# Optimization experiments

Hardware: AMD Instinct MI355X
Metric: run time of the kernel (lower is better)

## Reference

```python
import jax, jax.numpy as jnp
import numpy as np

B, L, D, K = 16, 2048, 128, 8192
NUM_RQ_STEPS = 1


def _nearest(residual, codebook):
    # residual: [B,L,D], codebook: [K,D]
    d2 = (
        jnp.sum(residual * residual, axis=-1, keepdims=True)  # [B,L,1]
        - 2.0 * jnp.einsum('bld,kd->blk', residual, codebook)  # [B,L,K]
        + jnp.sum(codebook * codebook, axis=-1)  # [K]
    )
    idx = jnp.argmin(d2, axis=-1)  # [B,L]
    return codebook[idx], idx  # gather: [B,L,D]


def setup_inputs() -> dict:
    key = jax.random.key(0)
    k1, k2 = jax.random.split(key)
    z_e = jax.random.normal(k1, (B, L, D), dtype=jnp.float32)
    codebook = jax.random.normal(k2, (K, D), dtype=jnp.float32)
    return {"z_e": z_e, "codebook": codebook}


def reference(z_e, codebook):
    # apply_codebook(z_e, code_sg=True): codebook is stop-gradiented,
    # residual quantization over NUM_RQ_STEPS, straight-through on output.
    cb = jax.lax.stop_gradient(codebook)
    residual = z_e
    z_q = jnp.zeros_like(z_e)
    idx_list = []
    for _ in range(NUM_RQ_STEPS):
        q, idx = _nearest(residual, cb)
        z_q = z_q + q
        residual = residual - q
        idx_list.append(idx)
    indices = jnp.stack(idx_list, axis=-1)  # [B,L,num_rq_steps]
    # straight-through estimator (code_sg=True): grads flow to z_e, not codebook
    z_q = z_e + jax.lax.stop_gradient(z_q - z_e)
    return z_q, indices
```

## Files before the change

### kernel.cpp

```cpp
#include <hip/hip_runtime.h>


#define M_TOK  32768
#define DIM    128
#define KCODES 8192
#define BM     64
#define NT     (KCODES / 256)
#define MARGIN 0.10f

typedef _Float16 half8v __attribute__((ext_vector_type(8)));
typedef float float4v __attribute__((ext_vector_type(4)));

union H2U { _Float16 h; unsigned short u; };
__device__ __forceinline__ unsigned short f2h_bits(_Float16 h) {
  H2U c; c.h = h; return c.u;
}

__device__ __forceinline__ void gload_lds16(const void* g, void* l) {
  __builtin_amdgcn_global_load_lds(
      (const __attribute__((address_space(1))) unsigned int*)g,
      (__attribute__((address_space(3))) unsigned int*)l, 16, 0, 0);
}

#define CNORM_OFF  (KCODES * 256)
#define QCNT_OFF   (CNORM_OFF + KCODES * 4)
#define QTOK_OFF   (QCNT_OFF + 64)
#define KMIN_OFF   (QTOK_OFF + M_TOK * 4)

__global__ __launch_bounds__(256) void prep_kernel(
    const float* __restrict__ cb, unsigned short* __restrict__ Cs,
    float* __restrict__ cnorm, int* __restrict__ qcnt) {
  if (blockIdx.x == 0 && threadIdx.x == 0) *qcnt = 0;
  const int k = blockIdx.x * 4 + (threadIdx.x >> 6);
  const int lane = threadIdx.x & 63;
  const float2 v = ((const float2*)(cb + (size_t)k * DIM))[lane];
  float s = v.x * v.x + v.y * v.y;
  #pragma unroll
  for (int off = 32; off > 0; off >>= 1) s += __shfl_down(s, off);
  if (lane == 0) cnorm[k] = s;
  ushort2 hi;
  hi.x = f2h_bits((_Float16)v.x);
  hi.y = f2h_bits((_Float16)v.y);
  *(ushort2*)(Cs + (size_t)k * 128 + lane * 2) = hi;
}

__global__ __launch_bounds__(256, 2) void vq_mfma_kernel(
    const float* __restrict__ ze, const unsigned short* __restrict__ Cs,
    const float* __restrict__ cnorm, const float* __restrict__ cb,
    int* __restrict__ qcnt, int* __restrict__ qtok,
    unsigned long long* __restrict__ kmin,
    float* __restrict__ out_zq, float* __restrict__ out_idx) {
  __shared__ char lds[49152];
  char* const As = lds;
  char* const Bs = lds + 16384;

  const int tid = threadIdx.x;
  const int wn = tid >> 6;
  const int lane = tid & 63;
  const int quad = lane >> 4;
  const int l15 = lane & 15;
  const int m0 = blockIdx.x * BM;

  int loffC[4];
  #pragma unroll
  for (int c = 0; c < 4; ++c) {
    const int r = c * 16 + (lane >> 2);
    const int s = lane & 3;
    const int seg = s ^ ((r >> 1) & 3);
    loffC[c] = (wn * 64 + r) * 256 + seg * 16;
  }
  int boff[4];
  #pragma unroll
  for (int j = 0; j < 4; ++j) {
    const int n = j * 16 + l15;
    boff[j] = n * 64 + ((quad ^ ((n >> 1) & 3)) << 4);
  }
  char* const BsW = Bs + wn * 8192;

  {
    const int r = tid >> 2;
    const int qh = tid & 3;
    const float* zrow = ze + (size_t)(m0 + r) * DIM + qh * 32;
    char* arow = As + r * 256;
    const int rx = r & 7;
    #pragma unroll
    for (int i = 0; i < 8; ++i) {
      const float4 v = *(const float4*)(zrow + i * 4);
      ushort4 hh;
      hh.x = f2h_bits((_Float16)v.x);
      hh.y = f2h_bits((_Float16)v.y);
      hh.z = f2h_bits((_Float16)v.z);
      hh.w = f2h_bits((_Float16)v.w);
      const int c = qh * 32 + i * 4;
      *(ushort4*)(arow + ((((c >> 3) ^ rx) << 4) | ((c & 7) << 1))) = hh;
    }
  }
  __syncthreads();

  half8v ahi[4][4];
  #pragma unroll
  for (int ks = 0; ks < 4; ++ks)
    #pragma unroll
    for (int i = 0; i < 4; ++i) {
      const int m = i * 16 + l15;
      const int kslot = ks * 4 + quad;
      ahi[ks][i] = *(const half8v*)(As + m * 256 + ((kslot ^ (m & 7)) << 4));
    }

  float bestv[16], secv[16], idxv[16];
  #pragma unroll
  for (int s = 0; s < 16; ++s) {
    bestv[s] = 3.4e38f; secv[s] = 3.4e38f; idxv[s] = 0.f;
  }

  for (int nt = 0; nt < NT; ++nt) {
    const char* const tile = (const char*)Cs + (size_t)nt * 65536;
    float cnv[4];
    #pragma unroll
    for (int j = 0; j < 4; ++j)
      cnv[j] = cnorm[nt * 256 + wn * 64 + j * 16 + l15];

    float4v acc[4][4];
    #pragma unroll
    for (int i = 0; i < 4; ++i)
      #pragma unroll
      for (int j = 0; j < 4; ++j) acc[i][j] = (float4v)0.0f;

    #pragma unroll
    for (int t = 0; t < 2; ++t) {
      __syncthreads();
      #pragma unroll
      for (int p = 0; p < 2; ++p)
        #pragma unroll
        for (int c = 0; c < 4; ++c)
          gload_lds16(tile + (t * 2 + p) * 64 + loffC[c],
                      BsW + p * 4096 + c * 1024);
      __syncthreads();

      #pragma unroll
      for (int p = 0; p < 2; ++p) {
        const int kk = t * 2 + p;
        half8v bf[4];
        #pragma unroll
        for (int j = 0; j < 4; ++j)
          bf[j] = *(const half8v*)(BsW + p * 4096 + boff[j]);
        #pragma unroll
        for (int i = 0; i < 4; ++i)
          #pragma unroll
          for (int j = 0; j < 4; ++j)
            acc[i][j] = __builtin_amdgcn_mfma_f32_16x16x32_f16(
                ahi[kk][i], bf[j], acc[i][j], 0, 0, 0);
      }
    }

    #pragma unroll
    for (int j = 0; j < 4; ++j) {
      const float nidx = (float)(nt * 256 + wn * 64 + j * 16 + l15);
      const float cn = cnv[j];
      #pragma unroll
      for (int i = 0; i < 4; ++i)
        #pragma unroll
        for (int rg = 0; rg < 4; ++rg) {
          const float sc = fmaf(-2.0f, acc[i][j][rg], cn);
          const int slot = i * 4 + rg;
          const bool bt = sc < bestv[slot];
          secv[slot] = bt ? bestv[slot] : fminf(secv[slot], sc);
          idxv[slot] = bt ? nidx : idxv[slot];
          bestv[slot] = bt ? sc : bestv[slot];
        }
    }
  }

  #pragma unroll
  for (int slot = 0; slot < 16; ++slot) {
    float b = bestv[slot], sec = secv[slot], ix = idxv[slot];
    #pragma unroll
    for (int mk = 1; mk <= 8; mk <<= 1) {
      const float ob = __shfl_xor(b, mk);
      const float os = __shfl_xor(sec, mk);
      const float oi = __shfl_xor(ix, mk);
      const bool take = (ob < b) || (ob == b && oi < ix);
      const float loser = take ? b : ob;
      b = take ? ob : b;
      ix = take ? oi : ix;
      sec = fminf(fminf(sec, os), loser);
    }
    bestv[slot] = b; secv[slot] = sec; idxv[slot] = ix;
  }

  __syncthreads();
  float* const redB = (float*)lds;
  float* const redS = redB + 256;
  float* const redI = redB + 512;
  float* const lidxs = redB + 768;
  if (l15 == 0) {
    #pragma unroll
    for (int slot = 0; slot < 16; ++slot) {
      const int row = (slot >> 2) * 16 + quad * 4 + (slot & 3);
      redB[wn * 64 + row] = bestv[slot];
      redS[wn * 64 + row] = secv[slot];
      redI[wn * 64 + row] = idxv[slot];
    }
  }
  __syncthreads();
  if (tid < 64) {
    float b = redB[tid], sec = redS[tid], ix = redI[tid];
    #pragma unroll
    for (int w = 1; w < 4; ++w) {
      const float ob = redB[w * 64 + tid];
      const float os = redS[w * 64 + tid];
      const float oi = redI[w * 64 + tid];
      const bool take = (ob < b) || (ob == b && oi < ix);
      const float loser = take ? b : ob;
      b = take ? ob : b;
      ix = take ? oi : ix;
      sec = fminf(fminf(sec, os), loser);
    }
    out_idx[m0 + tid] = ix;
    lidxs[tid] = ix;
    if (sec - b < MARGIN) {
      kmin[m0 + tid] = ~0ull;
      const int p = atomicAdd(qcnt, 1);
      qtok[p] = m0 + tid;
    }
  }
  __syncthreads();

  const int tl = tid >> 2, qp = tid & 3;
  const int code = (int)lidxs[tl];
  const float4* src = (const float4*)(cb + (size_t)code * DIM);
  float4* dst = (float4*)(out_zq + (size_t)(m0 + tl) * DIM);
  #pragma unroll
  for (int p = 0; p < 8; ++p) dst[qp + p * 4] = src[qp + p * 4];
}

__global__ __launch_bounds__(256) void rescan_part_kernel(
    const float* __restrict__ ze, const float* __restrict__ cb,
    const float* __restrict__ cnorm, const int* __restrict__ qcnt,
    const int* __restrict__ qtok, unsigned long long* __restrict__ kmin) {
  __shared__ float xsh[DIM];
  __shared__ float rs[256];
  __shared__ int ri[256];
  const int tid = threadIdx.x;
  const int chunk = blockIdx.x & 31;
  const int n = *qcnt;
  for (int qi = blockIdx.x >> 5; qi < n; qi += (gridDim.x >> 5)) {
    const int token = qtok[qi];
    __syncthreads();
    if (tid < 32)
      ((float4*)xsh)[tid] = ((const float4*)(ze + (size_t)token * DIM))[tid];
    __syncthreads();
    const int code = chunk * 256 + tid;
    const float* crow = cb + (size_t)code * DIM;
    float dot = 0.f;
    #pragma unroll
    for (int d = 0; d < DIM; ++d) dot = fmaf(xsh[d], crow[d], dot);
    rs[tid] = fmaf(-2.f, dot, cnorm[code]);
    ri[tid] = code;
    __syncthreads();
    #pragma unroll
    for (int off = 128; off > 0; off >>= 1) {
      if (tid < off) {
        const float so = rs[tid + off];
        const int io = ri[tid + off];
        if (so < rs[tid] || (so == rs[tid] && io < ri[tid])) {
          rs[tid] = so; ri[tid] = io;
        }
      }
      __syncthreads();
    }
    if (tid == 0) {
      union { float f; unsigned int u; } c; c.f = rs[0];
      const unsigned int m = (c.u >> 31) ? ~c.u : (c.u | 0x80000000u);
      const unsigned long long key =
          ((unsigned long long)m << 32) | (unsigned int)ri[0];
      atomicMin(&kmin[token], key);
    }
    __syncthreads();
  }
}

__global__ __launch_bounds__(256) void rescan_apply_kernel(
    const float* __restrict__ cb, const int* __restrict__ qcnt,
    const int* __restrict__ qtok, const unsigned long long* __restrict__ kmin,
    float* __restrict__ out_zq, float* __restrict__ out_idx) {
  const int tid = threadIdx.x;
  const int n = *qcnt;
  for (int qi = blockIdx.x; qi < n; qi += gridDim.x) {
    const int token = qtok[qi];
    const int code = (int)(unsigned int)(kmin[token] & 0xFFFFFFFFull);
    if (tid == 0) out_idx[token] = (float)code;
    if (tid < 32)
      ((float4*)(out_zq + (size_t)token * DIM))[tid] =
          ((const float4*)(cb + (size_t)code * DIM))[tid];
  }
}

extern "C" void kernel_launch(void* const* d_in, const int* in_sizes, int n_in,
                              void* d_out, int out_size, void* d_ws,
                              size_t ws_size, hipStream_t stream) {
  const float* ze = (const float*)d_in[0];
  const float* cb = (const float*)d_in[1];
  float* out = (float*)d_out;

  unsigned short* Cs = (unsigned short*)d_ws;
  float* cnorm = (float*)((char*)d_ws + CNORM_OFF);
  int* qcnt = (int*)((char*)d_ws + QCNT_OFF);
  int* qtok = (int*)((char*)d_ws + QTOK_OFF);
  unsigned long long* kmin = (unsigned long long*)((char*)d_ws + KMIN_OFF);

  prep_kernel<<<KCODES / 4, 256, 0, stream>>>(cb, Cs, cnorm, qcnt);
  vq_mfma_kernel<<<M_TOK / BM, 256, 0, stream>>>(
      ze, Cs, cnorm, cb, qcnt, qtok, kmin, out, out + (size_t)M_TOK * DIM);
  rescan_part_kernel<<<4096, 256, 0, stream>>>(ze, cb, cnorm, qcnt, qtok,
                                               kmin);
  rescan_apply_kernel<<<256, 256, 0, stream>>>(cb, qcnt, qtok, kmin, out,
                                               out + (size_t)M_TOK * DIM);
}
```

Measured before the change: 269.1 us.

## Split codebook scan into two chunks with a separate merge kernel

The main MFMA distance kernel now scans only half the codebook per block, using a 2D grid over token tiles and codebook chunks. Each block writes a partial (best, second-best, index) record to workspace, and a new merge kernel combines them, then does the margin check, enqueues tokens for rescan and gathers the output. LDS is cut by aliasing the A staging buffer with the B tiles, and launch bounds are raised to allow more resident blocks per CU. This doubles the grid for better occupancy and load balance, at the cost of reloading A per chunk, an extra launch and partial-record traffic.

```diff
diff --git a/kernel.cpp b/kernel.cpp
--- a/kernel.cpp
+++ b/kernel.cpp
@@ -5,7 +5,9 @@
 #define DIM    128
 #define KCODES 8192
 #define BM     64
-#define NT     (KCODES / 256)
+#define NCHUNK 2
+#define CHUNK  (KCODES / NCHUNK)
+#define NT     (CHUNK / 256)
 #define MARGIN 0.10f
 
 typedef _Float16 half8v __attribute__((ext_vector_type(8)));
@@ -26,6 +28,7 @@
 #define QCNT_OFF   (CNORM_OFF + KCODES * 4)
 #define QTOK_OFF   (QCNT_OFF + 64)
 #define KMIN_OFF   (QTOK_OFF + M_TOK * 4)
+#define PART_OFF   (KMIN_OFF + M_TOK * 8)
 
 __global__ __launch_bounds__(256) void prep_kernel(
     const float* __restrict__ cb, unsigned short* __restrict__ Cs,
@@ -44,15 +47,10 @@
   *(ushort2*)(Cs + (size_t)k * 128 + lane * 2) = hi;
 }
 
-__global__ __launch_bounds__(256, 2) void vq_mfma_kernel(
+__global__ __launch_bounds__(256, 4) void vq_mfma_kernel(
     const float* __restrict__ ze, const unsigned short* __restrict__ Cs,
-    const float* __restrict__ cnorm, const float* __restrict__ cb,
-    int* __restrict__ qcnt, int* __restrict__ qtok,
-    unsigned long long* __restrict__ kmin,
-    float* __restrict__ out_zq, float* __restrict__ out_idx) {
-  __shared__ char lds[49152];
-  char* const As = lds;
-  char* const Bs = lds + 16384;
+    const float* __restrict__ cnorm, float4* __restrict__ partials) {
+  __shared__ char lds[32768];
 
   const int tid = threadIdx.x;
   const int wn = tid >> 6;
@@ -60,6 +58,7 @@
   const int quad = lane >> 4;
   const int l15 = lane & 15;
   const int m0 = blockIdx.x * BM;
+  const int cbase = blockIdx.y * CHUNK;
 
   int loffC[4];
   #pragma unroll
@@ -75,9 +74,10 @@
     const int n = j * 16 + l15;
     boff[j] = n * 64 + ((quad ^ ((n >> 1) & 3)) << 4);
   }
-  char* const BsW = Bs + wn * 8192;
+  char* const BsW = lds + wn * 8192;
 
   {
+    char* const As = lds;
     const int r = tid >> 2;
     const int qh = tid & 3;
     const float* zrow = ze + (size_t)(m0 + r) * DIM + qh * 32;
@@ -104,8 +104,9 @@
     for (int i = 0; i < 4; ++i) {
       const int m = i * 16 + l15;
       const int kslot = ks * 4 + quad;
-      ahi[ks][i] = *(const half8v*)(As + m * 256 + ((kslot ^ (m & 7)) << 4));
-    }
+      ahi[ks][i] = *(const half8v*)(lds + m * 256 + ((kslot ^ (m & 7)) << 4));
+    }
+  __syncthreads();
 
   float bestv[16], secv[16], idxv[16];
   #pragma unroll
@@ -114,11 +115,11 @@
   }
 
   for (int nt = 0; nt < NT; ++nt) {
-    const char* const tile = (const char*)Cs + (size_t)nt * 65536;
+    const char* const tile = (const char*)Cs + (size_t)(cbase + nt * 256) * 256;
     float cnv[4];
     #pragma unroll
     for (int j = 0; j < 4; ++j)
-      cnv[j] = cnorm[nt * 256 + wn * 64 + j * 16 + l15];
+      cnv[j] = cnorm[cbase + nt * 256 + wn * 64 + j * 16 + l15];
 
     float4v acc[4][4];
     #pragma unroll
@@ -155,7 +156,7 @@
 
     #pragma unroll
     for (int j = 0; j < 4; ++j) {
-      const float nidx = (float)(nt * 256 + wn * 64 + j * 16 + l15);
+      const float nidx = (float)(cbase + nt * 256 + wn * 64 + j * 16 + l15);
       const float cn = cnv[j];
       #pragma unroll
       for (int i = 0; i < 4; ++i)
@@ -192,7 +193,6 @@
   float* const redB = (float*)lds;
   float* const redS = redB + 256;
   float* const redI = redB + 512;
-  float* const lidxs = redB + 768;
   if (l15 == 0) {
     #pragma unroll
     for (int slot = 0; slot < 16; ++slot) {
@@ -216,20 +216,45 @@
       ix = take ? oi : ix;
       sec = fminf(fminf(sec, os), loser);
     }
-    out_idx[m0 + tid] = ix;
+    partials[(size_t)blockIdx.y * M_TOK + m0 + tid] =
+        make_float4(b, sec, ix, 0.f);
+  }
+}
+
+__global__ __launch_bounds__(256) void merge_kernel(
+    const float* __restrict__ cb, const float4* __restrict__ partials,
+    int* __restrict__ qcnt, int* __restrict__ qtok,
+    unsigned long long* __restrict__ kmin,
+    float* __restrict__ out_zq, float* __restrict__ out_idx) {
+  __shared__ float lidxs[64];
+  const int tid = threadIdx.x;
+  const int t0 = blockIdx.x * 64;
+  if (tid < 64) {
+    const int token = t0 + tid;
+    float4 p = partials[token];
+    float b = p.x, sec = p.y, ix = p.z;
+    #pragma unroll
+    for (int c = 1; c < NCHUNK; ++c) {
+      const float4 q = partials[(size_t)c * M_TOK + token];
+      const bool take = (q.x < b) || (q.x == b && q.z < ix);
+      const float loser = take ? b : q.x;
+      b = take ? q.x : b;
+      ix = take ? q.z : ix;
+      sec = fminf(fminf(sec, q.y), loser);
+    }
+    out_idx[token] = ix;
     lidxs[tid] = ix;
     if (sec - b < MARGIN) {
-      kmin[m0 + tid] = ~0ull;
-      const int p = atomicAdd(qcnt, 1);
-      qtok[p] = m0 + tid;
-    }
-  }
-  __syncthreads();
-
+      kmin[token] = ~0ull;
+      const int p2 = atomicAdd(qcnt, 1);
+      qtok[p2] = token;
+    }
+  }
+  __syncthreads();
   const int tl = tid >> 2, qp = tid & 3;
   const int code = (int)lidxs[tl];
   const float4* src = (const float4*)(cb + (size_t)code * DIM);
-  float4* dst = (float4*)(out_zq + (size_t)(m0 + tl) * DIM);
+  float4* dst = (float4*)(out_zq + (size_t)(t0 + tl) * DIM);
   #pragma unroll
   for (int p = 0; p < 8; ++p) dst[qp + p * 4] = src[qp + p * 4];
 }
@@ -308,10 +333,13 @@
   int* qcnt = (int*)((char*)d_ws + QCNT_OFF);
   int* qtok = (int*)((char*)d_ws + QTOK_OFF);
   unsigned long long* kmin = (unsigned long long*)((char*)d_ws + KMIN_OFF);
+  float4* partials = (float4*)((char*)d_ws + PART_OFF);
 
   prep_kernel<<<KCODES / 4, 256, 0, stream>>>(cb, Cs, cnorm, qcnt);
-  vq_mfma_kernel<<<M_TOK / BM, 256, 0, stream>>>(
-      ze, Cs, cnorm, cb, qcnt, qtok, kmin, out, out + (size_t)M_TOK * DIM);
+  vq_mfma_kernel<<<dim3(M_TOK / BM, NCHUNK), 256, 0, stream>>>(
+      ze, Cs, cnorm, partials);
+  merge_kernel<<<M_TOK / 64, 256, 0, stream>>>(
+      cb, partials, qcnt, qtok, kmin, out, out + (size_t)M_TOK * DIM);
   rescan_part_kernel<<<4096, 256, 0, stream>>>(ze, cb, cnorm, qcnt, qtok,
                                                kmin);
   rescan_apply_kernel<<<256, 256, 0, stream>>>(cb, qcnt, qtok, kmin, out,
```

Result: slower. 603.8 us (+124.4%).

## Keep codebook slices in registers and reduce rescan with wave shuffles

Applied to the files above, without the earlier changes.

The exact-fp32 rescan kernel is restructured so each block owns a fixed 64-code chunk held in registers, and iterates over queued tokens in 4 strided splits. Dot products are split across 16 lanes and reduced with xor shuffles, and the argmin is done per wavefront with shuffles and one atomicMin per wave instead of LDS tree reductions with many barriers. This removes repeated codebook row reloads and shared-memory synchronisation per token, at the cost of more atomics and fewer blocks (512) when the queue is short.

```diff
diff --git a/kernel.cpp b/kernel.cpp
--- a/kernel.cpp
+++ b/kernel.cpp
@@ -238,45 +238,65 @@
     const float* __restrict__ ze, const float* __restrict__ cb,
     const float* __restrict__ cnorm, const int* __restrict__ qcnt,
     const int* __restrict__ qtok, unsigned long long* __restrict__ kmin) {
-  __shared__ float xsh[DIM];
-  __shared__ float rs[256];
-  __shared__ int ri[256];
   const int tid = threadIdx.x;
-  const int chunk = blockIdx.x & 31;
+  const int wn = tid >> 6;
+  const int lane = tid & 63;
+  const int cs = lane >> 4;
+  const int dl = lane & 15;
+  const int chunk = blockIdx.x & 127;
+  const int split = blockIdx.x >> 7;
   const int n = *qcnt;
-  for (int qi = blockIdx.x >> 5; qi < n; qi += (gridDim.x >> 5)) {
+  if (n == 0) return;
+
+  float4 ca[4], cbv[4];
+  float cn[4];
+  int codes[4];
+  #pragma unroll
+  for (int it = 0; it < 4; ++it) {
+    const int c = chunk * 64 + wn * 16 + it * 4 + cs;
+    codes[it] = c;
+    cn[it] = cnorm[c];
+    const float* crow = cb + (size_t)c * DIM + dl * 8;
+    ca[it] = *(const float4*)crow;
+    cbv[it] = *(const float4*)(crow + 4);
+  }
+
+  for (int qi = split; qi < n; qi += 4) {
     const int token = qtok[qi];
-    __syncthreads();
-    if (tid < 32)
-      ((float4*)xsh)[tid] = ((const float4*)(ze + (size_t)token * DIM))[tid];
-    __syncthreads();
-    const int code = chunk * 256 + tid;
-    const float* crow = cb + (size_t)code * DIM;
-    float dot = 0.f;
-    #pragma unroll
-    for (int d = 0; d < DIM; ++d) dot = fmaf(xsh[d], crow[d], dot);
-    rs[tid] = fmaf(-2.f, dot, cnorm[code]);
-    ri[tid] = code;
-    __syncthreads();
-    #pragma unroll
-    for (int off = 128; off > 0; off >>= 1) {
-      if (tid < off) {
-        const float so = rs[tid + off];
-        const int io = ri[tid + off];
-        if (so < rs[tid] || (so == rs[tid] && io < ri[tid])) {
-          rs[tid] = so; ri[tid] = io;
-        }
-      }
-      __syncthreads();
-    }
-    if (tid == 0) {
-      union { float f; unsigned int u; } c; c.f = rs[0];
+    const float* xrow = ze + (size_t)token * DIM + dl * 8;
+    const float4 xa = *(const float4*)xrow;
+    const float4 xb = *(const float4*)(xrow + 4);
+
+    float b = 3.4e38f;
+    int bi = 0;
+    #pragma unroll
+    for (int it = 0; it < 4; ++it) {
+      float p = xa.x * ca[it].x;
+      p = fmaf(xa.y, ca[it].y, p);
+      p = fmaf(xa.z, ca[it].z, p);
+      p = fmaf(xa.w, ca[it].w, p);
+      p = fmaf(xb.x, cbv[it].x, p);
+      p = fmaf(xb.y, cbv[it].y, p);
+      p = fmaf(xb.z, cbv[it].z, p);
+      p = fmaf(xb.w, cbv[it].w, p);
+      #pragma unroll
+      for (int mk = 1; mk <= 8; mk <<= 1) p += __shfl_xor(p, mk);
+      const float sc = fmaf(-2.f, p, cn[it]);
+      if (sc < b || (sc == b && codes[it] < bi)) { b = sc; bi = codes[it]; }
+    }
+    #pragma unroll
+    for (int mk = 16; mk <= 32; mk <<= 1) {
+      const float ob = __shfl_xor(b, mk);
+      const int oi = __shfl_xor(bi, mk);
+      if (ob < b || (ob == b && oi < bi)) { b = ob; bi = oi; }
+    }
+    if (lane == 0) {
+      union { float f; unsigned int u; } c; c.f = b;
       const unsigned int m = (c.u >> 31) ? ~c.u : (c.u | 0x80000000u);
       const unsigned long long key =
-          ((unsigned long long)m << 32) | (unsigned int)ri[0];
+          ((unsigned long long)m << 32) | (unsigned int)bi;
       atomicMin(&kmin[token], key);
     }
-    __syncthreads();
   }
 }
 
@@ -312,8 +332,8 @@
   prep_kernel<<<KCODES / 4, 256, 0, stream>>>(cb, Cs, cnorm, qcnt);
   vq_mfma_kernel<<<M_TOK / BM, 256, 0, stream>>>(
       ze, Cs, cnorm, cb, qcnt, qtok, kmin, out, out + (size_t)M_TOK * DIM);
-  rescan_part_kernel<<<4096, 256, 0, stream>>>(ze, cb, cnorm, qcnt, qtok,
-                                               kmin);
+  rescan_part_kernel<<<512, 256, 0, stream>>>(ze, cb, cnorm, qcnt, qtok,
+                                              kmin);
   rescan_apply_kernel<<<256, 256, 0, stream>>>(cb, qcnt, qtok, kmin, out,
                                                out + (size_t)M_TOK * DIM);
 }
```

Measured after the change: 345.5 us. +28.4%, slower.
